# Optimization experiments

Measured on AMD Instinct MI355X. Metric: run time of the kernel, lower is better.

## Reference

```python
import jax, jax.numpy as jnp
import numpy as np

EPS = 1e-5  # torch BatchNorm2d default eps


def _conv(x, w, b, pad):
    y = jax.lax.conv_general_dilated(
        x, w, window_strides=(1, 1), padding=[(pad, pad), (pad, pad)],
        dimension_numbers=('NCHW', 'OIHW', 'NCHW'))
    return y + b[None, :, None, None]


def _bn_train(x, gamma, beta):
    # training-mode BatchNorm2d: biased batch statistics over (N,H,W)
    m = jnp.mean(x, axis=(0, 2, 3), keepdims=True)
    v = jnp.var(x, axis=(0, 2, 3), keepdims=True)
    xn = (x - m) * jax.lax.rsqrt(v + EPS)
    return xn * gamma[None, :, None, None] + beta[None, :, None, None]


def _ncc(s, t):
    # Vectorized equivalent of the per-pixel double loop.
    # ncc[b,0,i,j] = mean(tt * ss / (tt_std * ss_std)) over (C,th,tw)
    #             = sum(tt * s_sub) / (N * tt_std * ss_std)   (since sum(tt)=0)
    b, c, sh, sw = s.shape
    th, tw = t.shape[2], t.shape[3]
    N = c * th * tw
    tt = t - jnp.mean(t, axis=(1, 2, 3), keepdims=True)
    # torch.std is unbiased (divides by N-1)
    tt_std = jnp.sqrt(jnp.sum(tt * tt, axis=(1, 2, 3), keepdims=True) / (N - 1))

    # cross[b] = valid correlation of s[b] with its own template tt[b]
    def per_sample(si, ti):
        return jax.lax.conv_general_dilated(
            si[None], ti[None], (1, 1), 'VALID',
            dimension_numbers=('NCHW', 'OIHW', 'NCHW'))[0]  # (1,h,w)

    cross = jax.vmap(per_sample)(s, tt)  # (b,1,h,w)

    # per-window mean/std of s via box-filter conv over all C channels jointly
    box = jnp.ones((1, c, th, tw), dtype=s.dtype)
    win_sum = jax.lax.conv_general_dilated(
        s, box, (1, 1), 'VALID', dimension_numbers=('NCHW', 'OIHW', 'NCHW'))
    win_sqsum = jax.lax.conv_general_dilated(
        s * s, box, (1, 1), 'VALID', dimension_numbers=('NCHW', 'OIHW', 'NCHW'))
    win_mean = win_sum / N
    ss_var = jnp.maximum(win_sqsum - N * win_mean * win_mean, 0.0) / (N - 1)
    ss_std = jnp.sqrt(ss_var)

    return cross / (N * tt_std * ss_std)  # (b,1,h,w)


def reference(s, t, w1, b1, g1, be1, w2, b2, g2, be2,
              w3, b3, g3, be3, w4, b4):
    s = _bn_train(_conv(s, w1, b1, pad=1), g1, be1)
    t = _bn_train(_conv(t, w2, b2, pad=1), g2, be2)
    ncc = _ncc(s, t)
    x = _bn_train(_conv(ncc, w3, b3, pad=0), g3, be3)
    x = jax.nn.relu(x)
    return _conv(x, w4, b4, pad=0)  # (b,2,h,w)


def setup_inputs() -> dict:
    key = jax.random.key(0)
    ks = jax.random.split(key, 12)
    C = 256
    inp = {
        's': jax.random.normal(ks[0], (16, C, 64, 64), jnp.float32),
        't': jax.random.normal(ks[1], (16, C, 16, 16), jnp.float32),
        'w1': jax.random.normal(ks[2], (C, C, 3, 3), jnp.float32) * 0.02,
        'b1': jax.random.normal(ks[3], (C,), jnp.float32) * 0.02,
        'g1': jnp.ones((C,), jnp.float32),
        'be1': jnp.zeros((C,), jnp.float32),
        'w2': jax.random.normal(ks[4], (C, C, 3, 3), jnp.float32) * 0.02,
        'b2': jax.random.normal(ks[5], (C,), jnp.float32) * 0.02,
        'g2': jnp.ones((C,), jnp.float32),
        'be2': jnp.zeros((C,), jnp.float32),
        'w3': jax.random.normal(ks[6], (1, 1, 1, 1), jnp.float32),
        'b3': jax.random.normal(ks[7], (1,), jnp.float32) * 0.02,
        'g3': jnp.ones((1,), jnp.float32),
        'be3': jnp.zeros((1,), jnp.float32),
        'w4': jax.random.normal(ks[8], (2, 1, 1, 1), jnp.float32),
        'b4': jax.random.normal(ks[9], (2,), jnp.float32) * 0.02,
    }
    return inp
```

## Files before the change

### kernel.cpp

```cpp
#include <hip/hip_runtime.h>
#include <hip/hip_bf16.h>

#define EPSV 1e-5f

constexpr int B_ = 16, C_ = 256;
constexpr int OHW_ = 49 * 49;
constexpr int NTOT = 256 * 16 * 16;
constexpr int GROUPS = 32, CPERG = 8;

typedef short bf16x8 __attribute__((ext_vector_type(8)));
typedef float f32x4 __attribute__((ext_vector_type(4)));

constexpr size_t OFF_S1 = 0;
constexpr size_t SZ_S1  = (size_t)16 * 256 * 4096;
constexpr size_t OFF_T2 = OFF_S1 + SZ_S1;
constexpr size_t SZ_T2  = (size_t)16 * 256 * 256;
constexpr size_t OFF_ST = OFF_T2 + SZ_T2;
constexpr size_t OFF_Z  = OFF_ST + 2048;
constexpr size_t OFF_C  = OFF_Z + 131072;
constexpr size_t SPC_BYTES = (size_t)16 * 66 * 66 * 256 * 2;
constexpr size_t TPC_BYTES = (size_t)16 * 18 * 18 * 256 * 2;
constexpr size_t WR_BYTES  = (size_t)9 * 256 * 256 * 2;
constexpr size_t CPOFF = 0;
constexpr size_t NCOFF = CPOFF + (size_t)GROUPS * 16 * OHW_;
constexpr size_t SATOFF = NCOFF + (size_t)16 * OHW_;

__device__ __forceinline__ void gload_lds16(const void* g, void* l) {
    __builtin_amdgcn_global_load_lds((const __attribute__((address_space(1))) unsigned int*)g,
                                     (__attribute__((address_space(3))) unsigned int*)l,
                                     16, 0, 0);
}

template<int W>
__device__ __forceinline__ void pad_body(int bid, const float* __restrict__ in,
                                         __hip_bfloat16* __restrict__ outp, float* tile)
{
    constexpr int PW = W + 2;
    int icg = bid & 3; bid >>= 2;
    int yp = bid % PW; bid /= PW;
    int b = bid;
    int ic0 = icg * 64;
    int tid = threadIdx.x;
    bool interior = (yp >= 1 && yp <= W);
    if (interior) {
        int y = yp - 1;
        for (int idx = tid; idx < 64 * W; idx += 256) {
            int i = idx / W, x = idx % W;
            tile[i * (W + 1) + x] = in[(((size_t)(b * C_ + ic0 + i)) * W + y) * W + x];
        }
    }
    __syncthreads();
    for (int idx = tid; idx < PW * 16; idx += 256) {
        int xp = idx >> 4, i4 = idx & 15;
        ushort4 v = make_ushort4(0, 0, 0, 0);
        if (interior && xp >= 1 && xp <= W) {
            #pragma unroll
            for (int k = 0; k < 4; ++k) {
                __hip_bfloat16 h = __float2bfloat16(tile[(i4 * 4 + k) * (W + 1) + xp - 1]);
                reinterpret_cast<unsigned short*>(&v)[k] = *reinterpret_cast<unsigned short*>(&h);
            }
        }
        *reinterpret_cast<ushort4*>(&outp[(((size_t)(b * PW) + yp) * PW + xp) * 256 + ic0 + i4 * 4]) = v;
    }
}

__global__ __launch_bounds__(256)
void pad_all(const float* __restrict__ s, const float* __restrict__ t,
             __hip_bfloat16* __restrict__ SPc, __hip_bfloat16* __restrict__ TPc,
             const float* __restrict__ w1, const float* __restrict__ w2,
             __hip_bfloat16* __restrict__ wr1, __hip_bfloat16* __restrict__ wr2)
{
    __shared__ float tile[64 * 65];
    constexpr int NP1 = 16 * 66 * 4, NP2 = 16 * 18 * 4;
    int bid = blockIdx.x;
    if (bid < NP1) { pad_body<64>(bid, s, SPc, tile); return; }
    bid -= NP1;
    if (bid < NP2) { pad_body<16>(bid, t, TPc, tile); return; }
    bid -= NP2;
    const float* w = (bid < 256) ? w1 : w2;
    __hip_bfloat16* wr = (bid < 256) ? wr1 : wr2;
    int idx = (bid & 255) * 256 + threadIdx.x;
    const float* src = w + (size_t)idx * 9;
    #pragma unroll
    for (int t_ = 0; t_ < 9; ++t_)
        wr[(size_t)t_ * 65536 + idx] = __float2bfloat16(src[t_]);
}

template<int W>
__device__ __forceinline__ void conv_body(
    int logical,
    const __hip_bfloat16* __restrict__ SPc, const __hip_bfloat16* __restrict__ Wr,
    const float* __restrict__ bias, float* __restrict__ out,
    float* __restrict__ csum, float* __restrict__ csq,
    __hip_bfloat16* A_lds, __hip_bfloat16* B_lds)
{
    constexpr int PW = W + 2;
    constexpr int NPIX = W * W;
    constexpr int NT = NPIX / 128;
    int nt = logical % NT; logical /= NT;
    int mt = logical & 1;  logical >>= 1;
    int b  = logical;
    int tid = threadIdx.x;
    int lane = tid & 63;
    int wv = tid >> 6, wm = wv >> 1, wn = wv & 1;
    int oc0 = mt * 128, p0 = nt * 128;

    f32x4 acc[4][4];
    #pragma unroll
    for (int i = 0; i < 4; ++i)
        #pragma unroll
        for (int j = 0; j < 4; ++j)
            #pragma unroll
            for (int r = 0; r < 4; ++r) acc[i][j][r] = 0.f;

    const bf16x8* Af = reinterpret_cast<const bf16x8*>(A_lds);
    const bf16x8* Bf = reinterpret_cast<const bf16x8*>(B_lds);
    int colb = lane >> 4;
    int rA = lane & 15;

    for (int kk = 0; kk < 36; ++kk) {
        __syncthreads();
        #pragma unroll
        for (int h = 0; h < 2; ++h) {
            int kc = kk * 2 + h;
            int tap = kc >> 3, icc = kc & 7;
            int ic0 = icc * 32;
            int dy = tap / 3, dx = tap - dy * 3;
            #pragma unroll
            for (int it = 0; it < 2; ++it) {
                int sIdx = tid + it * 256;
                int row = sIdx >> 2, seg = sIdx & 3;
                const __hip_bfloat16* srcA =
                    Wr + ((size_t)(tap * 256 + oc0 + row)) * 256 + ic0 + seg * 8;
                gload_lds16(srcA, &A_lds[h * 4096 + sIdx * 8]);
                int p = p0 + row;
                int y = p / W, x = p % W;
                const __hip_bfloat16* srcB =
                    SPc + (((size_t)(b * PW + y + dy)) * PW + x + dx) * 256 + ic0 + seg * 8;
                gload_lds16(srcB, &B_lds[h * 4096 + sIdx * 8]);
            }
        }
        asm volatile("s_waitcnt vmcnt(0)" ::: "memory");
        __syncthreads();

        #pragma unroll
        for (int h = 0; h < 2; ++h) {
            bf16x8 a[4], bb[4];
            #pragma unroll
            for (int mi = 0; mi < 4; ++mi)
                a[mi] = Af[h * 512 + (wm * 64 + mi * 16 + rA) * 4 + colb];
            #pragma unroll
            for (int ni = 0; ni < 4; ++ni)
                bb[ni] = Bf[h * 512 + (wn * 64 + ni * 16 + rA) * 4 + colb];
            #pragma unroll
            for (int mi = 0; mi < 4; ++mi)
                #pragma unroll
                for (int ni = 0; ni < 4; ++ni)
                    acc[mi][ni] = __builtin_amdgcn_mfma_f32_16x16x32_bf16(
                        a[mi], bb[ni], acc[mi][ni], 0, 0, 0);
        }
    }

    #pragma unroll
    for (int mi = 0; mi < 4; ++mi) {
        int ocb = oc0 + wm * 64 + mi * 16 + colb * 4;
        #pragma unroll
        for (int r = 0; r < 4; ++r) {
            int oc = ocb + r;
            float bv = bias[oc];
            float* orow = out + ((size_t)(b * C_ + oc)) * NPIX;
            float s_oc = 0.f, q_oc = 0.f;
            #pragma unroll
            for (int ni = 0; ni < 4; ++ni) {
                int px = p0 + wn * 64 + ni * 16 + rA;
                float v = acc[mi][ni][r] + bv;
                orow[px] = v;
                s_oc += v; q_oc += v * v;
            }
            #pragma unroll
            for (int m_ = 1; m_ < 16; m_ <<= 1) {
                s_oc += __shfl_xor(s_oc, m_);
                q_oc += __shfl_xor(q_oc, m_);
            }
            if (rA == 0) {
                atomicAdd(&csum[oc], s_oc);
                atomicAdd(&csq[oc], q_oc);
            }
        }
    }
}

__global__ __launch_bounds__(256)
void conv_all(const __hip_bfloat16* __restrict__ SPc, const __hip_bfloat16* __restrict__ Wr1,
              const float* __restrict__ b1, float* __restrict__ S1,
              float* __restrict__ CHS1, float* __restrict__ CHQ1,
              const __hip_bfloat16* __restrict__ TPc, const __hip_bfloat16* __restrict__ Wr2,
              const float* __restrict__ b2, float* __restrict__ T2,
              float* __restrict__ CHS2, float* __restrict__ CHQ2)
{
    __shared__ __hip_bfloat16 A_lds[8192];
    __shared__ __hip_bfloat16 B_lds[8192];
    int bid = blockIdx.x;
    if (bid < 64) {
        conv_body<16>(bid, TPc, Wr2, b2, T2, CHS2, CHQ2, A_lds, B_lds);
    } else {
        int l = bid - 64;
        int logical = (l & 7) * 128 + (l >> 3);
        conv_body<64>(logical, SPc, Wr1, b1, S1, CHS1, CHQ1, A_lds, B_lds);
    }
}

__device__ inline void blk_reduce2(float& a, float& q, int tid) {
    #pragma unroll
    for (int off = 32; off > 0; off >>= 1) {
        a += __shfl_down(a, off);
        q += __shfl_down(q, off);
    }
    __shared__ float ra[4], rq[4];
    if ((tid & 63) == 0) { ra[tid >> 6] = a; rq[tid >> 6] = q; }
    __syncthreads();
    if (tid == 0) { a = ra[0] + ra[1] + ra[2] + ra[3]; q = rq[0] + rq[1] + rq[2] + rq[3]; }
}

__global__ __launch_bounds__(256)
void bn_t2_stats(float* __restrict__ T2, const float* __restrict__ csum,
                 const float* __restrict__ csq, const float* __restrict__ g2,
                 const float* __restrict__ be2, float* __restrict__ tmean,
                 float* __restrict__ ttstd)
{
    __shared__ float SC[256], SH[256];
    int b = blockIdx.x, tid = threadIdx.x;
    {
        float m = csum[tid] * (1.f / 4096.f);
        float v = csq[tid] * (1.f / 4096.f) - m * m;
        float sc = rsqrtf(v + EPSV) * g2[tid];
        SC[tid] = sc; SH[tid] = be2[tid] - m * sc;
    }
    __syncthreads();
    float4* p = reinterpret_cast<float4*>(T2 + (size_t)b * NTOT);
    float s = 0.f, q = 0.f;
    for (int i4 = tid; i4 < NTOT / 4; i4 += 256) {
        int c = i4 >> 6;
        float sc = SC[c], sh = SH[c];
        float4 v = p[i4];
        v.x = v.x * sc + sh; v.y = v.y * sc + sh;
        v.z = v.z * sc + sh; v.w = v.w * sc + sh;
        s += v.x + v.y + v.z + v.w;
        q += v.x * v.x + v.y * v.y + v.z * v.z + v.w * v.w;
        p[i4] = v;
    }
    blk_reduce2(s, q, tid);
    if (tid == 0) {
        float m = s / (float)NTOT;
        tmean[b] = m;
        ttstd[b] = sqrtf(fmaxf(q - (float)NTOT * m * m, 0.f) / (float)(NTOT - 1));
    }
}

__global__ __launch_bounds__(256, 2)
void cross_v3(const float* __restrict__ s1, const float* __restrict__ t2,
              const float* __restrict__ csum, const float* __restrict__ csq,
              const float* __restrict__ g1, const float* __restrict__ be1,
              float* __restrict__ cpart, float* __restrict__ z)
{
    __shared__ float4 spl4[1024];
    __shared__ float tpl[256];
    __shared__ float red[4][64][49];

    int g = blockIdx.x & (GROUPS - 1);
    int b = blockIdx.x / GROUPS;
    int tid = threadIdx.x;
    int phase = tid >> 6;
    int lane = tid & 63;
    int i = lane;
    int i_ld = i < 49 ? i : 48;

    float acc[49];
    #pragma unroll
    for (int j = 0; j < 49; ++j) acc[j] = 0.f;
    float4 zs[4], zq[4];
    #pragma unroll
    for (int k = 0; k < 4; ++k) {
        zs[k] = make_float4(0.f, 0.f, 0.f, 0.f);
        zq[k] = make_float4(0.f, 0.f, 0.f, 0.f);
    }

    #pragma unroll 1
    for (int cc = 0; cc < CPERG; ++cc) {
        int c = g * CPERG + cc;
        float m = csum[c] * (1.f / 65536.f);
        float v = csq[c] * (1.f / 65536.f) - m * m;
        float sc = rsqrtf(v + EPSV) * g1[c];
        float sh = be1[c] - m * sc;
        __syncthreads();
        const float4* sp4 = reinterpret_cast<const float4*>(s1 + ((size_t)(b * C_ + c)) * 4096);
        #pragma unroll
        for (int k = 0; k < 4; ++k) {
            int gidx = tid + k * 256;
            float4 val = sp4[gidx];
            val.x = val.x * sc + sh; val.y = val.y * sc + sh;
            val.z = val.z * sc + sh; val.w = val.w * sc + sh;
            zs[k].x += val.x; zs[k].y += val.y; zs[k].z += val.z; zs[k].w += val.w;
            zq[k].x += val.x * val.x; zq[k].y += val.y * val.y;
            zq[k].z += val.z * val.z; zq[k].w += val.w * val.w;
            int row = gidx >> 4, jg = gidx & 15;
            spl4[row * 16 + (jg ^ (row & 7))] = val;
        }
        tpl[tid] = t2[((size_t)(b * C_ + c)) * 256 + tid];
        __syncthreads();
        #pragma unroll 1
        for (int tyl = 0; tyl < 4; ++tyl) {
            int ty = phase * 4 + tyl;
            int row = i_ld + ty;
            float r_[64];
            #pragma unroll
            for (int jg = 0; jg < 16; ++jg) {
                float4 v4 = spl4[row * 16 + (jg ^ (row & 7))];
                r_[jg * 4 + 0] = v4.x; r_[jg * 4 + 1] = v4.y;
                r_[jg * 4 + 2] = v4.z; r_[jg * 4 + 3] = v4.w;
            }
            float tt[16];
            const float4* tp4 = reinterpret_cast<const float4*>(&tpl[ty * 16]);
            #pragma unroll
            for (int k = 0; k < 4; ++k) {
                float4 tv = tp4[k];
                tt[k * 4 + 0] = tv.x; tt[k * 4 + 1] = tv.y;
                tt[k * 4 + 2] = tv.z; tt[k * 4 + 3] = tv.w;
            }
            #pragma unroll
            for (int tx = 0; tx < 16; ++tx)
                #pragma unroll
                for (int j = 0; j < 49; ++j)
                    acc[j] += tt[tx] * r_[j + tx];
        }
    }
    #pragma unroll
    for (int k = 0; k < 4; ++k) {
        int pxb = (tid + k * 256) * 4;
        float* zb  = z + (size_t)b * 4096 + pxb;
        float* z2b = z + 65536 + (size_t)b * 4096 + pxb;
        atomicAdd(&zb[0], zs[k].x);  atomicAdd(&zb[1], zs[k].y);
        atomicAdd(&zb[2], zs[k].z);  atomicAdd(&zb[3], zs[k].w);
        atomicAdd(&z2b[0], zq[k].x); atomicAdd(&z2b[1], zq[k].y);
        atomicAdd(&z2b[2], zq[k].z); atomicAdd(&z2b[3], zq[k].w);
    }
    __syncthreads();
    if (i < 49) {
        #pragma unroll
        for (int j = 0; j < 49; ++j) red[phase][i][j] = acc[j];
    }
    __syncthreads();
    float* dst = cpart + ((size_t)(g * B_ + b)) * OHW_;
    for (int e = tid; e < OHW_; e += 256) {
        int ii = e / 49, jj = e - ii * 49;
        dst[e] = red[0][ii][jj] + red[1][ii][jj] + red[2][ii][jj] + red[3][ii][jj];
    }
}

__global__ __launch_bounds__(256)
void sat_kernel(const float* __restrict__ zin, float* __restrict__ sat)
{
    __shared__ float t[65][66];
    int pl = blockIdx.x;
    int tid = threadIdx.x;
    const float* src = zin + (size_t)pl * 4096;
    for (int idx = tid; idx < 4096; idx += 256) {
        int y = idx >> 6, x = idx & 63;
        t[y + 1][x + 1] = src[idx];
    }
    for (int idx = tid; idx < 65; idx += 256) { t[0][idx] = 0.f; t[idx][0] = 0.f; }
    __syncthreads();
    if (tid < 64) {
        float run = 0.f;
        for (int x = 1; x <= 64; ++x) { run += t[tid + 1][x]; t[tid + 1][x] = run; }
    }
    __syncthreads();
    if (tid < 64) {
        float run = 0.f;
        for (int y = 1; y <= 64; ++y) { run += t[y][tid + 1]; t[y][tid + 1] = run; }
    }
    __syncthreads();
    float* dst = sat + (size_t)pl * 4225;
    for (int idx = tid; idx < 4225; idx += 256) {
        int r = idx / 65, c = idx % 65;
        dst[idx] = t[r][c];
    }
}

__global__ __launch_bounds__(256)
void ncc_kernel(const float* __restrict__ cpart, const float* __restrict__ sat,
                const float* __restrict__ tmean, const float* __restrict__ ttstd,
                float* __restrict__ ncc, float* __restrict__ s3)
{
    int idx = blockIdx.x * 256 + threadIdx.x;
    float val = 0.f;
    if (idx < B_ * OHW_) {
        int b = idx / OHW_, r = idx - b * OHW_;
        int i = r / 49, j = r - i * 49;
        float cr = 0.f;
        #pragma unroll 4
        for (int g = 0; g < GROUPS; ++g) cr += cpart[((size_t)(g * B_ + b)) * OHW_ + r];
        const float* sz = sat + (size_t)b * 4225;
        const float* sq = sat + (size_t)(16 + b) * 4225;
        int a00 = i * 65 + j, a01 = i * 65 + j + 16;
        int a10 = (i + 16) * 65 + j, a11 = (i + 16) * 65 + j + 16;
        float wsum = sz[a11] - sz[a01] - sz[a10] + sz[a00];
        float wq   = sq[a11] - sq[a01] - sq[a10] + sq[a00];
        float crosst = cr - tmean[b] * wsum;
        float ssvar = fmaxf(wq - wsum * wsum * (1.f / 65536.f), 0.f) * (1.f / 65535.f);
        float ssstd = sqrtf(ssvar);
        val = crosst / (65536.f * ttstd[b] * ssstd);
        ncc[idx] = val;
    }
    float s = val, q = val * val;
    blk_reduce2(s, q, threadIdx.x);
    if (threadIdx.x == 0) { atomicAdd(&s3[0], s); atomicAdd(&s3[1], q); }
}

__global__ __launch_bounds__(256)
void final_kernel(const float* __restrict__ ncc, const float* __restrict__ s3,
                  const float* __restrict__ w3, const float* __restrict__ b3,
                  const float* __restrict__ g3, const float* __restrict__ be3,
                  const float* __restrict__ w4, const float* __restrict__ b4,
                  float* __restrict__ out)
{
    int idx = blockIdx.x * 256 + threadIdx.x;
    if (idx >= B_ * OHW_) return;
    constexpr float M = (float)(B_ * OHW_);
    float mn = s3[0] / M;
    float vn = s3[1] / M - mn * mn;
    float W3 = w3[0], B3 = b3[0];
    float my = W3 * mn + B3;
    float vy = W3 * W3 * vn;
    float sc = rsqrtf(vy + EPSV) * g3[0];
    float y = (W3 * ncc[idx] + B3 - my) * sc + be3[0];
    float h = fmaxf(y, 0.f);
    int b = idx / OHW_, r = idx - b * OHW_;
    out[((size_t)(b * 2 + 0)) * OHW_ + r] = h * w4[0] + b4[0];
    out[((size_t)(b * 2 + 1)) * OHW_ + r] = h * w4[1] + b4[1];
}

extern "C" void kernel_launch(void* const* d_in, const int* in_sizes, int n_in,
                              void* d_out, int out_size, void* d_ws, size_t ws_size,
                              hipStream_t stream)
{
    const float* s   = (const float*)d_in[0];
    const float* t   = (const float*)d_in[1];
    const float* w1  = (const float*)d_in[2];
    const float* b1  = (const float*)d_in[3];
    const float* g1  = (const float*)d_in[4];
    const float* be1 = (const float*)d_in[5];
    const float* w2  = (const float*)d_in[6];
    const float* b2  = (const float*)d_in[7];
    const float* g2  = (const float*)d_in[8];
    const float* be2 = (const float*)d_in[9];
    const float* w3  = (const float*)d_in[10];
    const float* b3  = (const float*)d_in[11];
    const float* g3  = (const float*)d_in[12];
    const float* be3 = (const float*)d_in[13];
    const float* w4  = (const float*)d_in[14];
    const float* b4  = (const float*)d_in[15];

    float* ws = (float*)d_ws;
    float* S1 = ws + OFF_S1;
    float* T2 = ws + OFF_T2;
    float* ST = ws + OFF_ST;
    float* CHS1 = ST + 0;
    float* CHQ1 = ST + 256;
    float* CHS2 = ST + 512;
    float* CHQ2 = ST + 768;
    float* S3   = ST + 1024;
    float* TM   = ST + 1040;
    float* TSD  = ST + 1056;
    float* Z    = ws + OFF_Z;

    char* Cb = (char*)(ws + OFF_C);
    __hip_bfloat16* SPc = (__hip_bfloat16*)Cb;
    __hip_bfloat16* TPc = (__hip_bfloat16*)(Cb + SPC_BYTES);
    __hip_bfloat16* Wr1 = (__hip_bfloat16*)(Cb + SPC_BYTES + TPC_BYTES);
    __hip_bfloat16* Wr2 = (__hip_bfloat16*)(Cb + SPC_BYTES + TPC_BYTES + WR_BYTES);
    float* Cf = (float*)Cb;
    float* CP  = Cf + CPOFF;
    float* NC  = Cf + NCOFF;
    float* SAT = Cf + SATOFF;

    hipMemsetAsync(ST, 0, (2048 + 131072) * sizeof(float), stream);

    pad_all<<<dim3(16 * 66 * 4 + 16 * 18 * 4 + 512), dim3(256), 0, stream>>>(
        s, t, SPc, TPc, w1, w2, Wr1, Wr2);

    conv_all<<<dim3(64 + 1024), dim3(256), 0, stream>>>(SPc, Wr1, b1, S1, CHS1, CHQ1,
                                                        TPc, Wr2, b2, T2, CHS2, CHQ2);

    bn_t2_stats<<<dim3(16), dim3(256), 0, stream>>>(T2, CHS2, CHQ2, g2, be2, TM, TSD);

    cross_v3<<<dim3(16 * GROUPS), dim3(256), 0, stream>>>(S1, T2, CHS1, CHQ1, g1, be1, CP, Z);
    sat_kernel<<<dim3(32), dim3(256), 0, stream>>>(Z, SAT);
    ncc_kernel<<<dim3(151), dim3(256), 0, stream>>>(CP, SAT, TM, TSD, NC, S3);
    final_kernel<<<dim3(151), dim3(256), 0, stream>>>(NC, S3, w3, b3, g3, be3, w4, b4, (float*)d_out);
}
```

Measured before the change: 438.0 us.

## Prefetch next K-chunk into registers to overlap global loads with MFMA

Replaces the direct global-to-LDS loads with a register-staged software pipeline. The next K iteration's tiles are loaded into registers while the current chunk is consumed by MFMAs, then written to LDS at the start of the following iteration. Per-thread base pointers are also precomputed once, which removes the per-iteration div/mod address math. This is meant to hide global memory latency behind compute, at the cost of extra VGPRs (eight float4) and explicit LDS stores.

```diff
diff --git a/kernel.cpp b/kernel.cpp
--- a/kernel.cpp
+++ b/kernel.cpp
@@ -25,12 +25,6 @@
 constexpr size_t NCOFF = CPOFF + (size_t)GROUPS * 16 * OHW_;
 constexpr size_t SATOFF = NCOFF + (size_t)16 * OHW_;
 
-__device__ __forceinline__ void gload_lds16(const void* g, void* l) {
-    __builtin_amdgcn_global_load_lds((const __attribute__((address_space(1))) unsigned int*)g,
-                                     (__attribute__((address_space(3))) unsigned int*)l,
-                                     16, 0, 0);
-}
-
 template<int W>
 __device__ __forceinline__ void pad_body(int bid, const float* __restrict__ in,
                                          __hip_bfloat16* __restrict__ outp, float* tile)
@@ -118,29 +112,43 @@
     int colb = lane >> 4;
     int rA = lane & 15;
 
-    for (int kk = 0; kk < 36; ++kk) {
-        __syncthreads();
+    int srow = tid >> 2, sseg = tid & 3;
+    const __hip_bfloat16* baseA0 = Wr + ((size_t)(oc0 + srow)) * 256 + sseg * 8;
+    const __hip_bfloat16* baseA1 = baseA0 + (size_t)64 * 256;
+    int p_0 = p0 + srow,  y_0 = p_0 / W, x_0 = p_0 % W;
+    int p_1 = p0 + srow + 64, y_1 = p_1 / W, x_1 = p_1 % W;
+    const __hip_bfloat16* baseB0 = SPc + (((size_t)(b * PW + y_0)) * PW + x_0) * 256 + sseg * 8;
+    const __hip_bfloat16* baseB1 = SPc + (((size_t)(b * PW + y_1)) * PW + x_1) * 256 + sseg * 8;
+
+    float4 rg[8];
+    auto GLOAD = [&](int kk) {
         #pragma unroll
         for (int h = 0; h < 2; ++h) {
             int kc = kk * 2 + h;
             int tap = kc >> 3, icc = kc & 7;
-            int ic0 = icc * 32;
-            int dy = tap / 3, dx = tap - dy * 3;
-            #pragma unroll
-            for (int it = 0; it < 2; ++it) {
-                int sIdx = tid + it * 256;
-                int row = sIdx >> 2, seg = sIdx & 3;
-                const __hip_bfloat16* srcA =
-                    Wr + ((size_t)(tap * 256 + oc0 + row)) * 256 + ic0 + seg * 8;
-                gload_lds16(srcA, &A_lds[h * 4096 + sIdx * 8]);
-                int p = p0 + row;
-                int y = p / W, x = p % W;
-                const __hip_bfloat16* srcB =
-                    SPc + (((size_t)(b * PW + y + dy)) * PW + x + dx) * 256 + ic0 + seg * 8;
-                gload_lds16(srcB, &B_lds[h * 4096 + sIdx * 8]);
-            }
-        }
-        asm volatile("s_waitcnt vmcnt(0)" ::: "memory");
+            int offA = tap * 65536 + icc * 32;
+            int offB = ((tap / 3) * PW + (tap % 3)) * 256 + icc * 32;
+            rg[h * 4 + 0] = *reinterpret_cast<const float4*>(baseA0 + offA);
+            rg[h * 4 + 1] = *reinterpret_cast<const float4*>(baseA1 + offA);
+            rg[h * 4 + 2] = *reinterpret_cast<const float4*>(baseB0 + offB);
+            rg[h * 4 + 3] = *reinterpret_cast<const float4*>(baseB1 + offB);
+        }
+    };
+    auto WRITE = [&]() {
+        #pragma unroll
+        for (int h = 0; h < 2; ++h) {
+            *reinterpret_cast<float4*>(&A_lds[h * 4096 + tid * 8])        = rg[h * 4 + 0];
+            *reinterpret_cast<float4*>(&A_lds[h * 4096 + (tid + 256) * 8]) = rg[h * 4 + 1];
+            *reinterpret_cast<float4*>(&B_lds[h * 4096 + tid * 8])        = rg[h * 4 + 2];
+            *reinterpret_cast<float4*>(&B_lds[h * 4096 + (tid + 256) * 8]) = rg[h * 4 + 3];
+        }
+    };
+
+    GLOAD(0);
+    for (int kk = 0; kk < 36; ++kk) {
+        __syncthreads();
+        WRITE();
+        if (kk + 1 < 36) GLOAD(kk + 1);
         __syncthreads();
 
         #pragma unroll
```

New measurement: 637.2 us. 1.45x slower.
